# Optimization experiments

Hardware: AMD Instinct MI355X
Metric: run time of the kernel (lower is better)

The kernel has to match this reference:

```python
import jax, jax.numpy as jnp
import numpy as np

N_NODES = 100000


def setup_inputs() -> dict:
    key = jax.random.key(0)
    k1, k2, k3 = jax.random.split(key, 3)
    emb = jax.random.normal(k1, (N_NODES, 64), dtype=jnp.float32)
    src = jax.random.randint(k2, (1250000,), 0, N_NODES, dtype=jnp.int64)
    dst = jax.random.randint(k3, (1250000,), 0, N_NODES, dtype=jnp.int64)
    return {"emb": emb, "src": src, "dst": dst}


def reference(emb, src, dst):
    # DGL GraphConv(norm='both', weight=False, bias=False):
    #   out = D_in^{-1/2} * A * (D_out^{-1/2} * emb), degrees clamped to >= 1.
    n = emb.shape[0]
    e = src.shape[0]
    ones = jnp.ones((e,), dtype=emb.dtype)
    out_deg = jax.ops.segment_sum(ones, src, num_segments=n)  # out-degree of src nodes
    in_deg = jax.ops.segment_sum(ones, dst, num_segments=n)   # in-degree of dst nodes
    src_norm = jnp.clip(out_deg, 1.0, None) ** -0.5           # [N]
    dst_norm = jnp.clip(in_deg, 1.0, None) ** -0.5            # [N]
    h = emb * src_norm[:, None]                               # [N, D] pre-normalize
    msg = h[src]                                              # [E, D] gather
    agg = jax.ops.segment_sum(msg, dst, num_segments=n)       # [N, D] scatter-add
    return agg * dst_norm[:, None]
```

## Files before the change

kernel.cpp:

```cpp
#include <hip/hip_runtime.h>
#include <hip/hip_fp16.h>

#define NNODES 100000
#define DIM 64
#define TILE 128
#define NTILES ((NNODES + TILE - 1) / TILE)
#define NTPAD 784
#define CAP 2560
#define EPT 16
#define BIN_THREADS 512
#define BIN_CHUNK (BIN_THREADS * EPT)
#define NPAIR 4

__global__ __launch_bounds__(BIN_THREADS) void bin_kernel(
        const int* __restrict__ src, const int* __restrict__ dst,
        int* __restrict__ gcurD, int* __restrict__ gcurS,
        unsigned int* __restrict__ binnedD, unsigned char* __restrict__ binnedSb, int E) {
    __shared__ int histD[NTPAD], histS[NTPAD], baseD[NTPAD], baseS[NTPAD];
    __shared__ unsigned short rankD[BIN_CHUNK], rankS[BIN_CHUNK];
    int tid = threadIdx.x;
    for (int t = tid; t < NTPAD; t += BIN_THREADS) { histD[t] = 0; histS[t] = 0; }
    __syncthreads();
    int base = blockIdx.x * BIN_CHUNK;
    #pragma unroll
    for (int i = 0; i < EPT; i++) {
        int idx = base + i * BIN_THREADS + tid;
        if (idx < E) {
            int d = dst[idx];
            int s = src[idx];
            rankD[i * BIN_THREADS + tid] = (unsigned short)atomicAdd(&histD[d >> 7], 1);
            rankS[i * BIN_THREADS + tid] = (unsigned short)atomicAdd(&histS[s >> 7], 1);
        }
    }
    __syncthreads();
    for (int t = tid; t < NTPAD; t += BIN_THREADS) {
        int h = histD[t];
        baseD[t] = h ? atomicAdd(&gcurD[t], h) : 0;
        h = histS[t];
        baseS[t] = h ? atomicAdd(&gcurS[t], h) : 0;
    }
    __syncthreads();
    #pragma unroll
    for (int i = 0; i < EPT; i++) {
        int idx = base + i * BIN_THREADS + tid;
        if (idx < E) {
            int d = dst[idx];
            int s = src[idx];
            int tD = d >> 7, tS = s >> 7;
            int pD = baseD[tD] + (int)rankD[i * BIN_THREADS + tid];
            int pS = baseS[tS] + (int)rankS[i * BIN_THREADS + tid];
            if (pD < CAP) binnedD[(size_t)tD * CAP + pD] = ((unsigned)(d & 127) << 17) | (unsigned)s;
            if (pS < CAP) binnedSb[(size_t)tS * CAP + pS] = (unsigned char)(s & 127);
        }
    }
}

__global__ __launch_bounds__(256) void sortnorm_kernel(
        const int* __restrict__ gcurS, const unsigned char* __restrict__ binnedSb,
        const int* __restrict__ gcurD, const unsigned int* __restrict__ binnedD,
        const float* __restrict__ emb, __half* __restrict__ embp,
        int* __restrict__ sortedD, int* __restrict__ offs, int* __restrict__ deg) {
    __shared__ int cnt[TILE];
    __shared__ int cur[TILE];
    __shared__ float norm_s[TILE];
    __shared__ int wsum[2];
    __shared__ int tot_s;
    int t = blockIdx.x, tid = threadIdx.x;
    if (tid < TILE) cnt[tid] = 0;
    __syncthreads();
    {
        int lenS = min(gcurS[t], CAP);
        const unsigned char* segS = binnedSb + (size_t)t * CAP;
        for (int j = tid; j < lenS; j += 256)
            atomicAdd(&cnt[segS[j]], 1);
    }
    __syncthreads();
    if (tid < TILE)
        norm_s[tid] = rsqrtf(fmaxf((float)cnt[tid], 1.0f));
    __syncthreads();
    {
        int nrows = min(TILE, NNODES - t * TILE);
        int chunks = nrows * NPAIR;
        size_t ebase = (size_t)t * TILE * DIM;
        for (int i = tid; i < chunks; i += 256) {
            int row = i >> 2;
            int pair = i & 3;
            const float* ep = emb + ebase + (size_t)row * DIM + pair * 16;
            float w = norm_s[row];
            float4 a = *(const float4*)(ep);
            float4 b = *(const float4*)(ep + 4);
            float4 c = *(const float4*)(ep + 8);
            float4 d4 = *(const float4*)(ep + 12);
            int gnode = t * TILE + row;
            __half2* o = (__half2*)(embp + ((size_t)pair * (NNODES + 1) + gnode) * 16);
            o[0] = __floats2half2_rn(a.x * w, a.y * w);
            o[1] = __floats2half2_rn(a.z * w, a.w * w);
            o[2] = __floats2half2_rn(b.x * w, b.y * w);
            o[3] = __floats2half2_rn(b.z * w, b.w * w);
            o[4] = __floats2half2_rn(c.x * w, c.y * w);
            o[5] = __floats2half2_rn(c.z * w, c.w * w);
            o[6] = __floats2half2_rn(d4.x * w, d4.y * w);
            o[7] = __floats2half2_rn(d4.z * w, d4.w * w);
        }
        if (t * TILE + tid == NNODES) {
            __half2 z = __floats2half2_rn(0.0f, 0.0f);
            #pragma unroll
            for (int p = 0; p < NPAIR; p++) {
                __half2* o = (__half2*)(embp + ((size_t)p * (NNODES + 1) + NNODES) * 16);
                #pragma unroll
                for (int k = 0; k < 8; k++) o[k] = z;
            }
        }
    }
    __syncthreads();
    if (tid < TILE) cnt[tid] = 0;
    __syncthreads();
    int len = min(gcurD[t], CAP);
    const unsigned int* seg = binnedD + (size_t)t * CAP;
    for (int j = tid; j < len; j += 256)
        atomicAdd(&cnt[seg[j] >> 17], 1);
    __syncthreads();
    int v = 0, ex = 0;
    if (tid < TILE) {
        v = cnt[tid];
        int vpad = (v + 7) & ~7;
        int lane = tid & 63, w = tid >> 6;
        int x = vpad;
        #pragma unroll
        for (int off = 1; off < 64; off <<= 1) {
            int y = __shfl_up(x, off, 64);
            if (lane >= off) x += y;
        }
        if (lane == 63) wsum[w] = x;
        __syncthreads();
        int add = (w == 1) ? wsum[0] : 0;
        ex = x - vpad + add;
        cur[tid] = ex;
        if (tid == TILE - 1) tot_s = ex + vpad;
    } else {
        __syncthreads();
    }
    __syncthreads();
    for (int j = tid; j < len; j += 256) {
        unsigned int p = seg[j];
        int dl = p >> 17;
        int pos = atomicAdd(&cur[dl], 1);
        if (pos < CAP) sortedD[(size_t)t * CAP + pos] = (int)(p & 0x1FFFF);
    }
    __syncthreads();
    if (tid < TILE) {
        int vpad = (v + 7) & ~7;
        int pe = ex + vpad;
        for (int p = cur[tid]; p < pe && p < CAP; p++) sortedD[(size_t)t * CAP + p] = NNODES;
    }
    for (int k = tot_s + tid; k < CAP; k += 256) sortedD[(size_t)t * CAP + k] = NNODES;
    int node = t * TILE + tid;
    if (tid < TILE && node < NNODES) {
        offs[node] = t * CAP + ex;
        deg[node] = v;
    }
}

__global__ __launch_bounds__(256) void agg6_kernel(
        const __half* __restrict__ embp, const int* __restrict__ offs,
        const int* __restrict__ deg, const int* __restrict__ sortedD,
        float* __restrict__ out) {
    int bid = blockIdx.x;
    int pair = bid & 3;
    int g = bid >> 2;
    int wid = threadIdx.x >> 6;
    int lane = threadIdx.x & 63;
    int nodesub = lane >> 3;
    int slot = (lane >> 1) & 3;
    int hl = lane & 1;
    int node = g * 32 + wid * 8 + nodesub;
    if (node >= NNODES) return;
    int m = deg[node];
    int mp = (m + 7) & ~7;
    const int* run = sortedD + offs[node];
    const __half* tbl = embp + (size_t)pair * (NNODES + 1) * 16;
    __half2 hz = __floats2half2_rn(0.0f, 0.0f);
    __half2 h0 = hz, h1 = hz, h2 = hz, h3 = hz;
    for (int j = 0; j < mp; j += 8) {
        int i0 = run[j + slot];
        int i1 = run[j + 4 + slot];
        float4 v0 = *(const float4*)(tbl + ((size_t)i0 << 4) + (hl << 3));
        float4 v1 = *(const float4*)(tbl + ((size_t)i1 << 4) + (hl << 3));
        const __half2* p0 = (const __half2*)&v0;
        const __half2* p1 = (const __half2*)&v1;
        h0 = __hadd2(h0, p0[0]); h1 = __hadd2(h1, p0[1]);
        h2 = __hadd2(h2, p0[2]); h3 = __hadd2(h3, p0[3]);
        h0 = __hadd2(h0, p1[0]); h1 = __hadd2(h1, p1[1]);
        h2 = __hadd2(h2, p1[2]); h3 = __hadd2(h3, p1[3]);
    }
    float2 f0 = __half22float2(h0);
    float2 f1 = __half22float2(h1);
    float2 f2 = __half22float2(h2);
    float2 f3 = __half22float2(h3);
    float a0 = f0.x, a1 = f0.y, a2 = f1.x, a3 = f1.y;
    float a4 = f2.x, a5 = f2.y, a6 = f3.x, a7 = f3.y;
    #pragma unroll
    for (int off = 2; off <= 4; off <<= 1) {
        a0 += __shfl_xor(a0, off);
        a1 += __shfl_xor(a1, off);
        a2 += __shfl_xor(a2, off);
        a3 += __shfl_xor(a3, off);
        a4 += __shfl_xor(a4, off);
        a5 += __shfl_xor(a5, off);
        a6 += __shfl_xor(a6, off);
        a7 += __shfl_xor(a7, off);
    }
    float dn = rsqrtf(fmaxf((float)m, 1.0f));
    if (slot == 0) {
        float* op = out + ((size_t)node << 6) + (pair << 4) + (hl << 3);
        *(float4*)(op) = make_float4(a0 * dn, a1 * dn, a2 * dn, a3 * dn);
        *(float4*)(op + 4) = make_float4(a4 * dn, a5 * dn, a6 * dn, a7 * dn);
    }
}

extern "C" void kernel_launch(void* const* d_in, const int* in_sizes, int n_in,
                              void* d_out, int out_size, void* d_ws, size_t ws_size,
                              hipStream_t stream) {
    const float* emb = (const float*)d_in[0];
    const int* src = (const int*)d_in[1];
    const int* dst = (const int*)d_in[2];
    int E = in_sizes[1];
    float* out = (float*)d_out;

    int* gcurD = (int*)d_ws;
    int* gcurS = gcurD + NTPAD;
    unsigned int* binnedD = (unsigned int*)(gcurS + NTPAD);
    int* sortedD = (int*)(binnedD + (size_t)NTILES * CAP);
    unsigned char* binnedSb = (unsigned char*)(sortedD + (size_t)NTILES * CAP);
    int* offs = (int*)(binnedSb + (size_t)NTILES * CAP);
    int* deg = offs + NNODES;
    __half* embp = (__half*)(deg + NNODES);

    hipMemsetAsync(gcurD, 0, 2 * NTPAD * sizeof(int), stream);

    int bin_blocks = (E + BIN_CHUNK - 1) / BIN_CHUNK;
    bin_kernel<<<bin_blocks, BIN_THREADS, 0, stream>>>(src, dst, gcurD, gcurS, binnedD, binnedSb, E);

    sortnorm_kernel<<<NTILES, 256, 0, stream>>>(gcurS, binnedSb, gcurD, binnedD,
                                                emb, embp, sortedD, offs, deg);

    int ngroups = (NNODES + 31) / 32;
    agg6_kernel<<<ngroups * NPAIR, 256, 0, stream>>>(embp, offs, deg, sortedD, out);
}
```

Before: 92.28 us.

## Stage per-group neighbor index runs in LDS and halve binning chunk size

The aggregation kernel now has each 256-thread block copy the contiguous sorted-neighbor index span for its 32 nodes into shared memory with int4 loads. The gather loop then reads indices from LDS, falling back to global memory when the span exceeds the buffer. The aim is to replace scattered small global index reads with one coalesced bulk load. The cost is a 24 KB shared buffer that may lower occupancy, plus an extra barrier. Separately, the binning kernel processes 8 edges per thread instead of 16, which launches more, smaller blocks.

Result: slower. 96.22 us (+4.3%).

```diff
diff --git a/kernel.cpp b/kernel.cpp
--- a/kernel.cpp
+++ b/kernel.cpp
@@ -7,10 +7,12 @@
 #define NTILES ((NNODES + TILE - 1) / TILE)
 #define NTPAD 784
 #define CAP 2560
-#define EPT 16
+#define EPT 8
 #define BIN_THREADS 512
 #define BIN_CHUNK (BIN_THREADS * EPT)
 #define NPAIR 4
+#define GRP 32
+#define LDSCAP 6144
 
 __global__ __launch_bounds__(BIN_THREADS) void bin_kernel(
         const int* __restrict__ src, const int* __restrict__ dst,
@@ -161,23 +163,44 @@
     }
 }
 
-__global__ __launch_bounds__(256) void agg6_kernel(
+__global__ __launch_bounds__(256) void agg7_kernel(
         const __half* __restrict__ embp, const int* __restrict__ offs,
         const int* __restrict__ deg, const int* __restrict__ sortedD,
         float* __restrict__ out) {
+    __shared__ int runbuf[LDSCAP];
+    __shared__ int sh_base, sh_end;
     int bid = blockIdx.x;
     int pair = bid & 3;
     int g = bid >> 2;
-    int wid = threadIdx.x >> 6;
-    int lane = threadIdx.x & 63;
+    int node0 = g * GRP;
+    int tid = threadIdx.x;
+    if (tid == 0) {
+        sh_base = offs[node0];
+        int lastn = min(node0 + GRP - 1, NNODES - 1);
+        sh_end = offs[lastn] + ((deg[lastn] + 7) & ~7);
+    }
+    __syncthreads();
+    int base = sh_base;
+    int span = sh_end - base;
+    bool useLds = (span <= LDSCAP);
+    if (useLds) {
+        const int4* gsrc = (const int4*)(sortedD + base);
+        int4* ldst = (int4*)runbuf;
+        int n4 = span >> 2;
+        for (int i = tid; i < n4; i += 256) ldst[i] = gsrc[i];
+    }
+    __syncthreads();
+    int wid = tid >> 6;
+    int lane = tid & 63;
     int nodesub = lane >> 3;
     int slot = (lane >> 1) & 3;
     int hl = lane & 1;
-    int node = g * 32 + wid * 8 + nodesub;
+    int node = node0 + wid * 8 + nodesub;
     if (node >= NNODES) return;
     int m = deg[node];
     int mp = (m + 7) & ~7;
-    const int* run = sortedD + offs[node];
+    int roff = offs[node] - base;
+    const int* run = useLds ? (runbuf + roff) : (sortedD + base + roff);
     const __half* tbl = embp + (size_t)pair * (NNODES + 1) * 16;
     __half2 hz = __floats2half2_rn(0.0f, 0.0f);
     __half2 h0 = hz, h1 = hz, h2 = hz, h3 = hz;
@@ -244,6 +267,6 @@
     sortnorm_kernel<<<NTILES, 256, 0, stream>>>(gcurS, binnedSb, gcurD, binnedD,
                                                 emb, embp, sortedD, offs, deg);
 
-    int ngroups = (NNODES + 31) / 32;
-    agg6_kernel<<<ngroups * NPAIR, 256, 0, stream>>>(embp, offs, deg, sortedD, out);
-}
+    int ngroups = (NNODES + GRP - 1) / GRP;
+    agg7_kernel<<<ngroups * NPAIR, 256, 0, stream>>>(embp, offs, deg, sortedD, out);
+}
```
